# Kernel tuning notes

Hardware: AMD Instinct MI355X
Metric: run time of the kernel (lower is better)

Reference implementation:

```python
import jax, jax.numpy as jnp
import numpy as np

N_NODES = 100000
N_EDGES = 1600000
IN_DIM = 3
HID = 128


def setup_inputs() -> dict:
    key = jax.random.key(0)
    ks = jax.random.split(key, 16)
    s = 0.05
    inp = {
        "x": jax.random.normal(ks[0], (N_NODES, IN_DIM), dtype=jnp.float32),
        "pos": jax.random.normal(ks[1], (N_NODES, IN_DIM), dtype=jnp.float32),
        "edge_index": jax.random.randint(ks[2], (2, N_EDGES), 0, N_NODES, dtype=jnp.int64),
        # EdgeConv MLP: Linear(2*IN_DIM, HID) -> ReLU -> Linear(HID, HID)
        "w1": jax.random.normal(ks[3], (2 * IN_DIM, HID), dtype=jnp.float32) * s,
        "b1": jnp.zeros((HID,), dtype=jnp.float32),
        "w2": jax.random.normal(ks[4], (HID, HID), dtype=jnp.float32) * s,
        "b2": jnp.zeros((HID,), dtype=jnp.float32),
        # encoder tail: ReLU -> Linear(HID, HID)
        "w3": jax.random.normal(ks[5], (HID, HID), dtype=jnp.float32) * s,
        "b3": jnp.zeros((HID,), dtype=jnp.float32),
        # decoder: Linear(HID, HID) -> ReLU -> Linear(HID, 3)
        "w4": jax.random.normal(ks[6], (HID, HID), dtype=jnp.float32) * s,
        "b4": jnp.zeros((HID,), dtype=jnp.float32),
        "w5": jax.random.normal(ks[7], (HID, 3), dtype=jnp.float32) * s,
        "b5": jnp.zeros((3,), dtype=jnp.float32),
    }
    return inp


def reference(x, pos, edge_index, w1, b1, w2, b2, w3, b3, w4, b4, w5, b5):
    n = x.shape[0]
    src, dst = edge_index[0], edge_index[1]  # message j(src) -> i(dst)
    xi = x[dst]                               # [E, 3] target features
    xj = x[src]                               # [E, 3] source features
    msg_in = jnp.concatenate([xi, xj - xi], axis=-1)          # [E, 6]
    h = jax.nn.relu(msg_in @ w1 + b1) @ w2 + b2               # [E, HID]
    agg = jax.ops.segment_max(h, dst, num_segments=n)         # [N, HID]
    agg = jnp.where(jnp.isneginf(agg), 0.0, agg)              # nodes with no edges -> 0
    enc = jax.nn.relu(agg) @ w3 + b3                          # [N, HID]
    dec = jax.nn.relu(enc @ w4 + b4) @ w5 + b5                # [N, 3]
    return pos + 0.1 * jnp.tanh(dec)
```

## Files before the change

### kernel.cpp

```cpp
#include <hip/hip_runtime.h>
#include <hip/hip_bf16.h>

typedef __attribute__((ext_vector_type(8))) short short8;
typedef __attribute__((ext_vector_type(4))) float floatx4;
typedef __attribute__((ext_vector_type(2))) unsigned short ushortx2;

#define NHID 128
#define PADROW 136
#define EB 64
#define EB2 128
#define PB 256

__device__ __forceinline__ unsigned short f2bf(float x) {
  unsigned int u = __float_as_uint(x);
  u += 0x7FFFu + ((u >> 16) & 1u);
  return (unsigned short)(u >> 16);
}

__device__ __forceinline__ unsigned int pkbf(float a, float b) {
  __hip_bfloat162 h = __float22bfloat162_rn(make_float2(a, b));
  union { __hip_bfloat162 h; unsigned int u; } cv;
  cv.h = h;
  return cv.u;
}

__device__ __forceinline__ unsigned int pack2(float a, float b) {
  return (unsigned int)f2bf(a) | ((unsigned int)f2bf(b) << 16);
}

__device__ __forceinline__ unsigned int pkmax(unsigned int a, unsigned int b) {
  union { unsigned int u; ushortx2 v; } x, y;
  x.u = a; y.u = b;
  x.v = __builtin_elementwise_max(x.v, y.v);
  return x.u;
}

__device__ __forceinline__ void casmax(unsigned int* ap, unsigned int run) {
  unsigned int old = *ap;
  while (true) {
    unsigned int mx = pkmax(old, run);
    if (mx == old) break;
    unsigned int got = atomicCAS(ap, old, mx);
    if (got == old) break;
    old = got;
  }
}

__device__ __forceinline__ bool detect64(const int* __restrict__ ei) {
  unsigned long long b = __ballot(ei[2 * (threadIdx.x & 63) + 1] != 0);
  return b == 0ULL;
}

__device__ __forceinline__ void load_bfrags(const float* __restrict__ wmat,
                                            short8* bf, int m, int q) {
  #pragma unroll
  for (int kc = 0; kc < 4; ++kc) {
    #pragma unroll
    for (int nt = 0; nt < 8; ++nt) {
      short8 v;
      #pragma unroll
      for (int j = 0; j < 8; ++j)
        v[j] = (short)f2bf(wmat[(kc * 32 + q * 8 + j) * NHID + nt * 16 + m]);
      bf[kc * 8 + nt] = v;
    }
  }
}

__device__ __forceinline__ void load_bfrags_perm(const float* __restrict__ wmat,
                                                 short8* bf, int m, int q) {
  #pragma unroll
  for (int kc = 0; kc < 4; ++kc) {
    #pragma unroll
    for (int nt = 0; nt < 8; ++nt) {
      short8 v;
      #pragma unroll
      for (int j = 0; j < 8; ++j) {
        const int khw = kc * 32 + q * 8 + j;
        const int ctrue = ((khw & 7) << 4) | (khw >> 3);
        v[j] = (short)f2bf(wmat[ctrue * NHID + nt * 16 + m]);
      }
      bf[kc * 8 + nt] = v;
    }
  }
}

__device__ __forceinline__ void mfma_block(const unsigned short* uA,
                                           const short8* bf, floatx4* acc,
                                           int w, int m, int q) {
  #pragma unroll
  for (int kc = 0; kc < 4; ++kc) {
    short8 a = *(const short8*)(uA + (16 * w + m) * PADROW + kc * 32 + q * 8);
    #pragma unroll
    for (int nt = 0; nt < 8; ++nt)
      acc[nt] = __builtin_amdgcn_mfma_f32_16x16x32_bf16(a, bf[kc * 8 + nt],
                                                        acc[nt], 0, 0, 0);
  }
}

__global__ void zero_detect_kernel(float4* __restrict__ p, int n4,
                                   const int* __restrict__ ei, int* __restrict__ flag) {
  if (blockIdx.x == 0 && threadIdx.x < 64) {
    unsigned long long b = __ballot(ei[2 * threadIdx.x + 1] != 0);
    if (threadIdx.x == 0) flag[0] = (b == 0ULL) ? 1 : 0;
  }
  int i = blockIdx.x * blockDim.x + threadIdx.x;
  int stride = gridDim.x * blockDim.x;
  float4 z = make_float4(0.f, 0.f, 0.f, 0.f);
  for (; i < n4; i += stride) p[i] = z;
}


__global__ __launch_bounds__(256) void part_hist(const int* __restrict__ ei,
                                                 int* __restrict__ mat, int E, int nbuck,
                                                 float4* __restrict__ aggz, int n4) {
  const int bl = blockIdx.x, t = threadIdx.x;
  if (bl >= PB) {
    int i = (bl - PB) * 256 + t;
    const int st = (gridDim.x - PB) * 256;
    float4 z = make_float4(0.f, 0.f, 0.f, 0.f);
    for (; i < n4; i += st) aggz[i] = z;
    return;
  }
  __shared__ int hist[512];
  const bool is64 = detect64(ei);
  for (int i = t; i < nbuck; i += 256) hist[i] = 0;
  __syncthreads();
  const int chunk = (E + PB - 1) / PB;
  const int lo = bl * chunk;
  const int hi = min(lo + chunk, E);
  for (int i = lo + t; i < hi; i += 256) {
    int d = is64 ? ei[2 * E + 2 * i] : ei[E + i];
    atomicAdd(&hist[d >> 8], 1);
  }
  __syncthreads();
  for (int bu = t; bu < nbuck; bu += 256) mat[bu * PB + bl] = hist[bu];
}

__global__ __launch_bounds__(256) void scan_rows(int* __restrict__ mat,
                                                 int* __restrict__ btot, int nbuck) {
  __shared__ int sh[256];
  const int bu = blockIdx.x, t = threadIdx.x;
  const int v = mat[bu * PB + t];
  sh[t] = v;
  __syncthreads();
  for (int off = 1; off < 256; off <<= 1) {
    int x = (t >= off) ? sh[t - off] : 0;
    __syncthreads();
    sh[t] += x;
    __syncthreads();
  }
  mat[bu * PB + t] = sh[t] - v;
  if (t == 255) btot[bu] = sh[255];
}

__global__ __launch_bounds__(512) void scan_buckets(const int* __restrict__ btot,
                                                    int* __restrict__ bstart, int nbuck) {
  __shared__ int sh[512];
  const int t = threadIdx.x;
  const int v = (t < nbuck) ? btot[t] : 0;
  sh[t] = v;
  __syncthreads();
  for (int off = 1; off < 512; off <<= 1) {
    int x = (t >= off) ? sh[t - off] : 0;
    __syncthreads();
    sh[t] += x;
    __syncthreads();
  }
  if (t <= nbuck) bstart[t] = sh[t] - v;
}

__global__ __launch_bounds__(256) void part_scatter(const int* __restrict__ ei,
                                                    const int* __restrict__ mat,
                                                    const int* __restrict__ bstart,
                                                    int2* __restrict__ mid, int E, int nbuck) {
  __shared__ int off[512];
  const bool is64 = detect64(ei);
  const int bl = blockIdx.x, t = threadIdx.x;
  for (int bu = t; bu < nbuck; bu += 256) off[bu] = bstart[bu] + mat[bu * PB + bl];
  __syncthreads();
  const int chunk = (E + PB - 1) / PB;
  const int lo = bl * chunk;
  const int hi = min(lo + chunk, E);
  for (int i = lo + t; i < hi; i += 256) {
    int s = is64 ? ei[2 * i]         : ei[i];
    int d = is64 ? ei[2 * E + 2 * i] : ei[E + i];
    int p = atomicAdd(&off[d >> 8], 1);
    mid[p] = make_int2(s, d);
  }
}

__global__ __launch_bounds__(256) void bucket_sort(const int2* __restrict__ mid,
                                                   const int* __restrict__ bstart,
                                                   int2* __restrict__ sorted) {
  __shared__ int h[256], cnt[256];
  const int bu = blockIdx.x, t = threadIdx.x;
  const int lo = bstart[bu], hi = bstart[bu + 1];
  h[t] = 0; cnt[t] = 0;
  __syncthreads();
  for (int i = lo + t; i < hi; i += 256) atomicAdd(&h[mid[i].y & 255], 1);
  __syncthreads();
  const int v = h[t];
  for (int off = 1; off < 256; off <<= 1) {
    int x = (t >= off) ? h[t - off] : 0;
    __syncthreads();
    h[t] += x;
    __syncthreads();
  }
  const int excl = h[t] - v;
  __syncthreads();
  h[t] = excl;
  __syncthreads();
  for (int i = lo + t; i < hi; i += 256) {
    int2 e = mid[i];
    const int dl = e.y & 255;
    const int p = lo + h[dl] + atomicAdd(&cnt[dl], 1);
    sorted[p] = e;
  }
}


__global__ __launch_bounds__(512, 2) void edge_sorted_kernel(
    const float* __restrict__ x, const int2* __restrict__ sorted,
    const float* __restrict__ w1, const float* __restrict__ b1,
    const float* __restrict__ w2, const float* __restrict__ b2,
    unsigned int* aggu, int N, int E) {
  __shared__ unsigned short us[EB2 * PADROW];
  __shared__ short8 w2f[2048];
  __shared__ int esS[EB2], edS[EB2];
  __shared__ int pn[2];
  __shared__ unsigned long long maskS[2];
  __shared__ unsigned int pmS[8][64];

  const int t = threadIdx.x;
  const int lane = t & 63;
  const int w = t >> 6;
  const int m = lane & 15;
  const int q = lane >> 4;

  float b1c[8], b2c[8];
  #pragma unroll
  for (int nt = 0; nt < 8; ++nt) { b1c[nt] = b1[nt * 16 + m]; b2c[nt] = b2[nt * 16 + m]; }

  short8 bf1[8];
  #pragma unroll
  for (int nt = 0; nt < 8; ++nt) {
    short8 v;
    #pragma unroll
    for (int j = 0; j < 8; ++j)
      v[j] = (q == 0 && j < 6) ? (short)f2bf(w1[j * NHID + nt * 16 + m]) : (short)0;
    bf1[nt] = v;
  }

  for (int idx = t; idx < 2048; idx += 512) {
    const int fg = idx >> 6, ln = idx & 63;
    const int mm = ln & 15;
    const int kc = fg >> 3, nt = fg & 7;
    short8 v;
    #pragma unroll
    for (int j = 0; j < 8; ++j) {
      const int khw = kc * 32 + (ln >> 4) * 8 + j;
      const int ctrue = ((khw & 7) << 4) | (khw >> 3);
      v[j] = (short)f2bf(w2[ctrue * NHID + nt * 16 + mm]);
    }
    w2f[idx] = v;
  }

  const int jc = t & 63;
  const int quarter = t >> 6;

  const int nbt = (E + EB2 - 1) / EB2;
  __syncthreads();

  int2 sv = make_int2(0, -1);
  {
    const int tile0 = blockIdx.x;
    const int gb = tile0 * EB2;
    if (t < EB2) {
      const int e = gb + t;
      if (tile0 < nbt && e < E) sv = sorted[e];
    } else if (t == EB2) {
      sv.y = (tile0 < nbt && gb > 0) ? sorted[gb - 1].y : -2;
    } else if (t == EB2 + 1) {
      sv.y = (tile0 < nbt && gb + EB2 < E) ? sorted[gb + EB2].y : -2;
    }
  }

  for (int tile = blockIdx.x; tile < nbt; tile += gridDim.x) {
    if (t < EB2) { esS[t] = sv.x; edS[t] = sv.y; }
    else if (t == EB2) pn[0] = sv.y;
    else if (t == EB2 + 1) pn[1] = sv.y;
    __syncthreads();

    if (w == 0) {
      int d0 = edS[lane];
      int dp0 = (lane == 0) ? -9 : edS[lane - 1];
      unsigned long long mk0 = __ballot(lane == 0 || d0 != dp0);
      int d1 = edS[64 + lane];
      int dp1 = edS[63 + lane];
      unsigned long long mk1 = __ballot(d1 != dp1);
      if (lane == 0) { maskS[0] = mk0; maskS[1] = mk1; }
    }

    floatx4 acc[8];
    #pragma unroll
    for (int nt = 0; nt < 8; ++nt) { floatx4 z = {0.f, 0.f, 0.f, 0.f}; acc[nt] = z; }
    short8 a1 = {0, 0, 0, 0, 0, 0, 0, 0};
    if (q == 0) {
      const int e = 16 * w + m;
      const int si = esS[e];
      const int d0 = edS[e];
      const int di = (d0 < 0) ? 0 : d0;
      float xi0 = x[di * 3], xi1 = x[di * 3 + 1], xi2 = x[di * 3 + 2];
      float dd0 = x[si * 3] - xi0, dd1 = x[si * 3 + 1] - xi1, dd2 = x[si * 3 + 2] - xi2;
      union { short8 s; uint4 u; } cv;
      cv.u = make_uint4(pkbf(xi0, xi1), pkbf(xi2, dd0), pkbf(dd1, dd2), 0u);
      a1 = cv.s;
    }
    #pragma unroll
    for (int nt = 0; nt < 8; ++nt)
      acc[nt] = __builtin_amdgcn_mfma_f32_16x16x32_bf16(a1, bf1[nt], acc[nt], 0, 0, 0);

    #pragma unroll
    for (int r = 0; r < 4; ++r) {
      union { short8 s; uint4 u; } cv;
      cv.u = make_uint4(
        pkbf(fmaxf(acc[0][r] + b1c[0], 0.f), fmaxf(acc[1][r] + b1c[1], 0.f)),
        pkbf(fmaxf(acc[2][r] + b1c[2], 0.f), fmaxf(acc[3][r] + b1c[3], 0.f)),
        pkbf(fmaxf(acc[4][r] + b1c[4], 0.f), fmaxf(acc[5][r] + b1c[5], 0.f)),
        pkbf(fmaxf(acc[6][r] + b1c[6], 0.f), fmaxf(acc[7][r] + b1c[7], 0.f)));
      *(short8*)(&us[(16 * w + q * 4 + r) * PADROW + m * 8]) = cv.s;
    }
    __syncthreads();

    #pragma unroll
    for (int nt = 0; nt < 8; ++nt) { floatx4 z = {0.f, 0.f, 0.f, 0.f}; acc[nt] = z; }
    #pragma unroll
    for (int kc = 0; kc < 4; ++kc) {
      short8 a = *(const short8*)(&us[(16 * w + m) * PADROW + kc * 32 + q * 8]);
      #pragma unroll
      for (int nt = 0; nt < 8; ++nt)
        acc[nt] = __builtin_amdgcn_mfma_f32_16x16x32_bf16(a, w2f[(kc * 8 + nt) * 64 + lane],
                                                          acc[nt], 0, 0, 0);
    }
    __syncthreads();

    #pragma unroll
    for (int r = 0; r < 4; ++r) {
      union { short8 s; uint4 u; } cv;
      cv.u = make_uint4(
        pkbf(fmaxf(acc[0][r] + b2c[0], 0.f), fmaxf(acc[1][r] + b2c[1], 0.f)),
        pkbf(fmaxf(acc[2][r] + b2c[2], 0.f), fmaxf(acc[3][r] + b2c[3], 0.f)),
        pkbf(fmaxf(acc[4][r] + b2c[4], 0.f), fmaxf(acc[5][r] + b2c[5], 0.f)),
        pkbf(fmaxf(acc[6][r] + b2c[6], 0.f), fmaxf(acc[7][r] + b2c[7], 0.f)));
      *(short8*)(&us[(16 * w + q * 4 + r) * PADROW + m * 8]) = cv.s;
    }
    __syncthreads();

    {
      const int tn = tile + gridDim.x;
      const int gb = tn * EB2;
      int2 nv = make_int2(0, -1);
      if (t < EB2) {
        const int e = gb + t;
        if (tn < nbt && e < E) nv = sorted[e];
      } else if (t == EB2) {
        nv.y = (tn < nbt && gb > 0) ? sorted[gb - 1].y : -2;
      } else if (t == EB2 + 1) {
        nv.y = (tn < nbt && gb + EB2 < E) ? sorted[gb + EB2].y : -2;
      }
      sv = nv;
    }

    int os = -1, onxt = 0, od = -1; unsigned int opart = 0;
    {
      const unsigned long long mk0 = maskS[0], mk1 = maskS[1];
      const int prevd = pn[0], nextd = pn[1];
      const int r0 = quarter * 16, r1 = r0 + 16;
      const unsigned int* us32 = (const unsigned int*)us;
      int s;
      if (r0 < 64) {
        s = 63 - __builtin_clzll(mk0 & (~0ULL >> (63 - r0)));
      } else {
        unsigned long long hm = mk1 & (~0ULL >> (127 - r0));
        s = hm ? 127 - __builtin_clzll(hm) : 63 - __builtin_clzll(mk0);
      }
      while (s < r1) {
        int nxt;
        if (s < 63) {
          unsigned long long ab = mk0 & (~0ULL << (s + 1));
          if (ab) nxt = __builtin_ffsll((long long)ab) - 1;
          else    nxt = mk1 ? 64 + __builtin_ffsll((long long)mk1) - 1 : 128;
        } else if (s == 63) {
          nxt = mk1 ? 64 + __builtin_ffsll((long long)mk1) - 1 : 128;
        } else if (s < 127) {
          unsigned long long ab = mk1 & (~0ULL << (s - 63));
          nxt = ab ? 64 + __builtin_ffsll((long long)ab) - 1 : 128;
        } else nxt = 128;

        const int lo = (s > r0) ? s : r0;
        const int hi = (nxt < r1) ? nxt : r1;
        unsigned int run = 0;
        for (int r = lo; r < hi; ++r)
          run = pkmax(run, us32[r * (PADROW >> 1) + jc]);

        if (s < r0) {
          pmS[quarter][jc] = run;
        } else if (nxt <= r1) {
          const int d = edS[s];
          if (d >= 0) {
            const bool bnd = (s == 0 && prevd == d) || (nxt == 128 && nextd == d);
            unsigned int* ap = aggu + (size_t)d * 64 + jc;
            if (!bnd) *ap = run;
            else if (run) casmax(ap, run);
          }
        } else {
          os = s; onxt = nxt; od = edS[s]; opart = run;
        }
        s = nxt;
      }
    }
    __syncthreads();

    if (os >= 0 && od >= 0) {
      const int endq = (onxt - 1) >> 4;
      #pragma unroll 4
      for (int qq = quarter + 1; qq <= endq; ++qq)
        opart = pkmax(opart, pmS[qq][jc]);
      const bool bnd = (os == 0 && pn[0] == od) || (onxt == 128 && pn[1] == od);
      unsigned int* ap = aggu + (size_t)od * 64 + jc;
      if (!bnd) *ap = opart;
      else if (opart) casmax(ap, opart);
    }
    __syncthreads();
  }
}


__global__ __launch_bounds__(256, 2) void edge_atomic_kernel(
    const float* __restrict__ x, const int* __restrict__ ei,
    const float* __restrict__ w1, const float* __restrict__ b1,
    const float* __restrict__ w2, const float* __restrict__ b2,
    unsigned int* aggu, const int* __restrict__ flag64, int N, int E) {
  __shared__ unsigned short uA[EB * PADROW];
  __shared__ float w1s[6 * NHID];
  __shared__ float b1s[NHID], b2s[NHID];
  __shared__ int es[EB], ed[EB];

  const int t = threadIdx.x;
  const int lane = t & 63;
  const int w = t >> 6;
  const int m = lane & 15;
  const int q = lane >> 4;

  for (int i = t; i < 6 * NHID; i += 256) w1s[i] = w1[i];
  if (t < NHID) { b1s[t] = b1[t]; b2s[t] = b2[t]; }

  short8 bf[32];
  load_bfrags(w2, bf, m, q);

  const bool is64 = (flag64[0] != 0);
  const int nb = (E + EB - 1) / EB;

  for (int batch = blockIdx.x; batch < nb; batch += gridDim.x) {
    const int gbase = batch * EB;
    if (t < EB) {
      int e = gbase + t;
      es[t] = (e < E) ? (is64 ? ei[2 * e] : ei[e]) : 0;
    } else if (t < 2 * EB) {
      int tt = t - EB;
      int e = gbase + tt;
      ed[tt] = (e < E) ? (is64 ? ei[2 * E + 2 * e] : ei[E + e]) : 0;
    }
    __syncthreads();
    {
      const int e = t >> 2;
      const int c0 = (t & 3) * 32;
      const int si = es[e], di = ed[e];
      float xi0 = x[di * 3], xi1 = x[di * 3 + 1], xi2 = x[di * 3 + 2];
      float msg[6];
      msg[0] = xi0; msg[1] = xi1; msg[2] = xi2;
      msg[3] = x[si * 3] - xi0; msg[4] = x[si * 3 + 1] - xi1; msg[5] = x[si * 3 + 2] - xi2;
      unsigned int* d32 = (unsigned int*)uA;
      const int base32 = (e * PADROW + c0) >> 1;
      #pragma unroll
      for (int cc = 0; cc < 32; cc += 2) {
        float u0 = b1s[c0 + cc], u1 = b1s[c0 + cc + 1];
        #pragma unroll
        for (int d = 0; d < 6; ++d) {
          u0 += msg[d] * w1s[d * NHID + c0 + cc];
          u1 += msg[d] * w1s[d * NHID + c0 + cc + 1];
        }
        d32[base32 + (cc >> 1)] = pack2(fmaxf(u0, 0.f), fmaxf(u1, 0.f));
      }
    }
    __syncthreads();

    floatx4 acc[8];
    #pragma unroll
    for (int nt = 0; nt < 8; ++nt) { floatx4 z = {0.f, 0.f, 0.f, 0.f}; acc[nt] = z; }
    mfma_block(uA, bf, acc, w, m, q);

    #pragma unroll
    for (int nt = 0; nt < 8; ++nt) {
      const int c = nt * 16 + m;
      const float bb = b2s[c];
      const int kst = m * 8 + nt;
      #pragma unroll
      for (int r = 0; r < 4; ++r) {
        const int erow = 16 * w + q * 4 + r;
        if (gbase + erow < E) {
          float hb = acc[nt][r] + bb;
          if (hb > 0.f) {
            unsigned int v = (unsigned int)f2bf(hb);
            casmax(aggu + (size_t)ed[erow] * 64 + (kst >> 1), v << (16 * (kst & 1)));
          }
        }
      }
    }
    __syncthreads();
  }
}


__global__ __launch_bounds__(256, 2) void encdec_kernel(
    const float* __restrict__ w3, const float* __restrict__ b3,
    const float* __restrict__ w4, const float* __restrict__ b4,
    const float* __restrict__ w5, const float* __restrict__ b5,
    const float* __restrict__ pos, const unsigned short* __restrict__ agg16,
    float* __restrict__ out, int N) {
  __shared__ unsigned short uA[EB * PADROW];
  __shared__ short8 w4f[2048];
  __shared__ float w5s[NHID * 3];

  const int t = threadIdx.x;
  const int lane = t & 63;
  const int w = t >> 6;
  const int m = lane & 15;
  const int q = lane >> 4;

  float b3c[8], b4c[8];
  #pragma unroll
  for (int nt = 0; nt < 8; ++nt) { b3c[nt] = b3[nt * 16 + m]; b4c[nt] = b4[nt * 16 + m]; }

  short8 bf3[32];
  load_bfrags_perm(w3, bf3, m, q);

  for (int idx = t; idx < 2048; idx += 256) {
    const int fg = idx >> 6, ln = idx & 63;
    const int mm = ln & 15;
    const int kc = fg >> 3, nt = fg & 7;
    short8 v;
    #pragma unroll
    for (int j = 0; j < 8; ++j) {
      const int khw = kc * 32 + (ln >> 4) * 8 + j;
      const int ctrue = ((khw & 7) << 4) | (khw >> 3);
      v[j] = (short)f2bf(w4[ctrue * NHID + nt * 16 + mm]);
    }
    w4f[idx] = v;
  }
  for (int i = t; i < NHID * 3; i += 256) w5s[i] = w5[i];
  const float b50 = b5[0], b51 = b5[1], b52 = b5[2];

  const int ch = t & 15;
  const int rr = t >> 4;
  const int nb = (N + EB - 1) / EB;
  __syncthreads();

  uint4 rv[4];
  const uint4 uz = make_uint4(0u, 0u, 0u, 0u);
  {
    const int b0 = blockIdx.x;
    #pragma unroll
    for (int k = 0; k < 4; ++k) {
      const int node = b0 * EB + rr + 16 * k;
      rv[k] = (b0 < nb && node < N) ? ((const uint4*)agg16)[(size_t)node * 16 + ch] : uz;
    }
  }

  for (int batch = blockIdx.x; batch < nb; batch += gridDim.x) {
    const int base = batch * EB;
    #pragma unroll
    for (int k = 0; k < 4; ++k)
      *(uint4*)(&uA[(rr + 16 * k) * PADROW + ch * 8]) = rv[k];
    __syncthreads();

    {
      const int nxb = batch + gridDim.x;
      #pragma unroll
      for (int k = 0; k < 4; ++k) {
        const int node = nxb * EB + rr + 16 * k;
        rv[k] = (nxb < nb && node < N) ? ((const uint4*)agg16)[(size_t)node * 16 + ch] : uz;
      }
    }

    floatx4 acc[8];
    #pragma unroll
    for (int nt = 0; nt < 8; ++nt) { floatx4 z = {0.f, 0.f, 0.f, 0.f}; acc[nt] = z; }
    mfma_block(uA, bf3, acc, w, m, q);
    __syncthreads();

    #pragma unroll
    for (int r = 0; r < 4; ++r) {
      union { short8 s; uint4 u; } cv;
      cv.u = make_uint4(
        pkbf(acc[0][r] + b3c[0], acc[1][r] + b3c[1]),
        pkbf(acc[2][r] + b3c[2], acc[3][r] + b3c[3]),
        pkbf(acc[4][r] + b3c[4], acc[5][r] + b3c[5]),
        pkbf(acc[6][r] + b3c[6], acc[7][r] + b3c[7]));
      *(short8*)(&uA[(16 * w + q * 4 + r) * PADROW + m * 8]) = cv.s;
    }
    __syncthreads();

    #pragma unroll
    for (int nt = 0; nt < 8; ++nt) { floatx4 z = {0.f, 0.f, 0.f, 0.f}; acc[nt] = z; }
    #pragma unroll
    for (int kc = 0; kc < 4; ++kc) {
      short8 a = *(const short8*)(&uA[(16 * w + m) * PADROW + kc * 32 + q * 8]);
      #pragma unroll
      for (int nt = 0; nt < 8; ++nt)
        acc[nt] = __builtin_amdgcn_mfma_f32_16x16x32_bf16(a, w4f[(kc * 8 + nt) * 64 + lane],
                                                          acc[nt], 0, 0, 0);
    }

    float p[4][3];
    #pragma unroll
    for (int r = 0; r < 4; ++r) { p[r][0] = 0.f; p[r][1] = 0.f; p[r][2] = 0.f; }
    #pragma unroll
    for (int nt = 0; nt < 8; ++nt) {
      const int c = nt * 16 + m;
      const float bb = b4c[nt];
      const float w50 = w5s[c * 3], w51 = w5s[c * 3 + 1], w52 = w5s[c * 3 + 2];
      #pragma unroll
      for (int r = 0; r < 4; ++r) {
        float tv = fmaxf(acc[nt][r] + bb, 0.f);
        p[r][0] += tv * w50; p[r][1] += tv * w51; p[r][2] += tv * w52;
      }
    }
    #pragma unroll
    for (int off = 8; off >= 1; off >>= 1) {
      #pragma unroll
      for (int r = 0; r < 4; ++r) {
        p[r][0] += __shfl_xor(p[r][0], off, 16);
        p[r][1] += __shfl_xor(p[r][1], off, 16);
        p[r][2] += __shfl_xor(p[r][2], off, 16);
      }
    }
    if (m == 0) {
      #pragma unroll
      for (int r = 0; r < 4; ++r) {
        const int node = base + 16 * w + q * 4 + r;
        if (node < N) {
          out[node * 3]     = pos[node * 3]     + 0.1f * tanhf(p[r][0] + b50);
          out[node * 3 + 1] = pos[node * 3 + 1] + 0.1f * tanhf(p[r][1] + b51);
          out[node * 3 + 2] = pos[node * 3 + 2] + 0.1f * tanhf(p[r][2] + b52);
        }
      }
    }
    __syncthreads();
  }
}

extern "C" void kernel_launch(void* const* d_in, const int* in_sizes, int n_in,
                              void* d_out, int out_size, void* d_ws, size_t ws_size,
                              hipStream_t stream) {
  const float* x   = (const float*)d_in[0];
  const float* pos = (const float*)d_in[1];
  const int*   ei  = (const int*)d_in[2];
  const float* w1  = (const float*)d_in[3];
  const float* b1  = (const float*)d_in[4];
  const float* w2  = (const float*)d_in[5];
  const float* b2  = (const float*)d_in[6];
  const float* w3  = (const float*)d_in[7];
  const float* b3  = (const float*)d_in[8];
  const float* w4  = (const float*)d_in[9];
  const float* b4  = (const float*)d_in[10];
  const float* w5  = (const float*)d_in[11];
  const float* b5  = (const float*)d_in[12];
  float* out = (float*)d_out;

  const int N = in_sizes[0] / 3;
  const int E = in_sizes[2] / 2;
  const int nbuck = (N + 255) >> 8;

  char* ws = (char*)d_ws;
  unsigned short* agg16 = (unsigned short*)ws;
  const size_t aggB = (size_t)N * NHID * sizeof(unsigned short);
  int2* mid    = (int2*)(ws + aggB);
  int2* sorted = (int2*)(ws + aggB + (size_t)E * 8);
  int*  mat    = (int*)(ws + aggB + (size_t)E * 16);
  int*  btot   = mat + (size_t)nbuck * PB;
  int*  bstart = btot + nbuck;
  int*  flag   = bstart + nbuck + 2;
  const size_t needed = aggB + (size_t)E * 16 + ((size_t)nbuck * PB + 2 * nbuck + 8) * 4;

  if (ws_size >= needed && nbuck <= 511 && E >= 64) {
    part_hist<<<2048, 256, 0, stream>>>(ei, mat, E, nbuck, (float4*)agg16, N * 16);
    scan_rows<<<nbuck, 256, 0, stream>>>(mat, btot, nbuck);
    scan_buckets<<<1, 512, 0, stream>>>(btot, bstart, nbuck);
    part_scatter<<<PB, 256, 0, stream>>>(ei, mat, bstart, mid, E, nbuck);
    bucket_sort<<<nbuck, 256, 0, stream>>>(mid, bstart, sorted);
    edge_sorted_kernel<<<512, 512, 0, stream>>>(x, sorted, w1, b1, w2, b2,
                                                (unsigned int*)agg16, N, E);
  } else {
    int* flag2 = (int*)(ws + aggB);
    zero_detect_kernel<<<2048, 256, 0, stream>>>((float4*)agg16, N * 16, ei, flag2);
    edge_atomic_kernel<<<512, 256, 0, stream>>>(x, ei, w1, b1, w2, b2,
                                                (unsigned int*)agg16, flag2, N, E);
  }
  encdec_kernel<<<512, 256, 0, stream>>>(w3, b3, w4, b4, w5, b5, pos, agg16, out, N);
}
```

Before: 354.2 us.

## Fuse bucket scan into scatter, drop intra-wave barriers, seed accumulators with bias

After: 420.7 us. +18.8%, slower.

```diff
diff --git a/kernel.cpp b/kernel.cpp
--- a/kernel.cpp
+++ b/kernel.cpp
@@ -153,30 +153,34 @@
   if (t == 255) btot[bu] = sh[255];
 }
 
-__global__ __launch_bounds__(512) void scan_buckets(const int* __restrict__ btot,
-                                                    int* __restrict__ bstart, int nbuck) {
-  __shared__ int sh[512];
-  const int t = threadIdx.x;
-  const int v = (t < nbuck) ? btot[t] : 0;
-  sh[t] = v;
-  __syncthreads();
-  for (int off = 1; off < 512; off <<= 1) {
-    int x = (t >= off) ? sh[t - off] : 0;
-    __syncthreads();
-    sh[t] += x;
-    __syncthreads();
-  }
-  if (t <= nbuck) bstart[t] = sh[t] - v;
-}
-
 __global__ __launch_bounds__(256) void part_scatter(const int* __restrict__ ei,
                                                     const int* __restrict__ mat,
-                                                    const int* __restrict__ bstart,
+                                                    const int* __restrict__ btot,
+                                                    int* __restrict__ bstart,
                                                     int2* __restrict__ mid, int E, int nbuck) {
   __shared__ int off[512];
+  __shared__ int bsS[512];
   const bool is64 = detect64(ei);
   const int bl = blockIdx.x, t = threadIdx.x;
-  for (int bu = t; bu < nbuck; bu += 256) off[bu] = bstart[bu] + mat[bu * PB + bl];
+  const int o0 = (t < nbuck) ? btot[t] : 0;
+  const int o1 = (t + 256 < nbuck) ? btot[t + 256] : 0;
+  bsS[t] = o0; bsS[t + 256] = o1;
+  __syncthreads();
+  for (int o = 1; o < 256; o <<= 1) {
+    int x0 = (t >= o) ? bsS[t - o] : 0;
+    int x1 = (t >= o) ? bsS[256 + t - o] : 0;
+    __syncthreads();
+    bsS[t] += x0; bsS[256 + t] += x1;
+    __syncthreads();
+  }
+  const int tot0 = bsS[255];
+  bsS[256 + t] += tot0;
+  __syncthreads();
+  const int ex0 = bsS[t] - o0;
+  const int ex1 = bsS[256 + t] - o1;
+  if (bl == 0) { bstart[t] = ex0; bstart[256 + t] = ex1; }
+  off[t]       = ex0 + ((t < nbuck) ? mat[t * PB + bl] : 0);
+  off[256 + t] = ex1 + ((t + 256 < nbuck) ? mat[(t + 256) * PB + bl] : 0);
   __syncthreads();
   const int chunk = (E + PB - 1) / PB;
   const int lo = bl * chunk;
@@ -291,6 +295,21 @@
     else if (t == EB2 + 1) pn[1] = sv.y;
     __syncthreads();
 
+    {
+      const int tn = tile + gridDim.x;
+      const int gb = tn * EB2;
+      int2 nv = make_int2(0, -1);
+      if (t < EB2) {
+        const int e = gb + t;
+        if (tn < nbt && e < E) nv = sorted[e];
+      } else if (t == EB2) {
+        nv.y = (tn < nbt && gb > 0) ? sorted[gb - 1].y : -2;
+      } else if (t == EB2 + 1) {
+        nv.y = (tn < nbt && gb + EB2 < E) ? sorted[gb + EB2].y : -2;
+      }
+      sv = nv;
+    }
+
     if (w == 0) {
       int d0 = edS[lane];
       int dp0 = (lane == 0) ? -9 : edS[lane - 1];
@@ -303,7 +322,10 @@
 
     floatx4 acc[8];
     #pragma unroll
-    for (int nt = 0; nt < 8; ++nt) { floatx4 z = {0.f, 0.f, 0.f, 0.f}; acc[nt] = z; }
+    for (int nt = 0; nt < 8; ++nt) {
+      floatx4 z = {b1c[nt], b1c[nt], b1c[nt], b1c[nt]};
+      acc[nt] = z;
+    }
     short8 a1 = {0, 0, 0, 0, 0, 0, 0, 0};
     if (q == 0) {
       const int e = 16 * w + m;
@@ -324,16 +346,18 @@
     for (int r = 0; r < 4; ++r) {
       union { short8 s; uint4 u; } cv;
       cv.u = make_uint4(
-        pkbf(fmaxf(acc[0][r] + b1c[0], 0.f), fmaxf(acc[1][r] + b1c[1], 0.f)),
-        pkbf(fmaxf(acc[2][r] + b1c[2], 0.f), fmaxf(acc[3][r] + b1c[3], 0.f)),
-        pkbf(fmaxf(acc[4][r] + b1c[4], 0.f), fmaxf(acc[5][r] + b1c[5], 0.f)),
-        pkbf(fmaxf(acc[6][r] + b1c[6], 0.f), fmaxf(acc[7][r] + b1c[7], 0.f)));
+        pkbf(fmaxf(acc[0][r], 0.f), fmaxf(acc[1][r], 0.f)),
+        pkbf(fmaxf(acc[2][r], 0.f), fmaxf(acc[3][r], 0.f)),
+        pkbf(fmaxf(acc[4][r], 0.f), fmaxf(acc[5][r], 0.f)),
+        pkbf(fmaxf(acc[6][r], 0.f), fmaxf(acc[7][r], 0.f)));
       *(short8*)(&us[(16 * w + q * 4 + r) * PADROW + m * 8]) = cv.s;
     }
-    __syncthreads();
-
-    #pragma unroll
-    for (int nt = 0; nt < 8; ++nt) { floatx4 z = {0.f, 0.f, 0.f, 0.f}; acc[nt] = z; }
+
+    #pragma unroll
+    for (int nt = 0; nt < 8; ++nt) {
+      floatx4 z = {b2c[nt], b2c[nt], b2c[nt], b2c[nt]};
+      acc[nt] = z;
+    }
     #pragma unroll
     for (int kc = 0; kc < 4; ++kc) {
       short8 a = *(const short8*)(&us[(16 * w + m) * PADROW + kc * 32 + q * 8]);
@@ -342,34 +366,18 @@
         acc[nt] = __builtin_amdgcn_mfma_f32_16x16x32_bf16(a, w2f[(kc * 8 + nt) * 64 + lane],
                                                           acc[nt], 0, 0, 0);
     }
-    __syncthreads();
 
     #pragma unroll
     for (int r = 0; r < 4; ++r) {
       union { short8 s; uint4 u; } cv;
       cv.u = make_uint4(
-        pkbf(fmaxf(acc[0][r] + b2c[0], 0.f), fmaxf(acc[1][r] + b2c[1], 0.f)),
-        pkbf(fmaxf(acc[2][r] + b2c[2], 0.f), fmaxf(acc[3][r] + b2c[3], 0.f)),
-        pkbf(fmaxf(acc[4][r] + b2c[4], 0.f), fmaxf(acc[5][r] + b2c[5], 0.f)),
-        pkbf(fmaxf(acc[6][r] + b2c[6], 0.f), fmaxf(acc[7][r] + b2c[7], 0.f)));
+        pkbf(fmaxf(acc[0][r], 0.f), fmaxf(acc[1][r], 0.f)),
+        pkbf(fmaxf(acc[2][r], 0.f), fmaxf(acc[3][r], 0.f)),
+        pkbf(fmaxf(acc[4][r], 0.f), fmaxf(acc[5][r], 0.f)),
+        pkbf(fmaxf(acc[6][r], 0.f), fmaxf(acc[7][r], 0.f)));
       *(short8*)(&us[(16 * w + q * 4 + r) * PADROW + m * 8]) = cv.s;
     }
     __syncthreads();
-
-    {
-      const int tn = tile + gridDim.x;
-      const int gb = tn * EB2;
-      int2 nv = make_int2(0, -1);
-      if (t < EB2) {
-        const int e = gb + t;
-        if (tn < nbt && e < E) nv = sorted[e];
-      } else if (t == EB2) {
-        nv.y = (tn < nbt && gb > 0) ? sorted[gb - 1].y : -2;
-      } else if (t == EB2 + 1) {
-        nv.y = (tn < nbt && gb + EB2 < E) ? sorted[gb + EB2].y : -2;
-      }
-      sv = nv;
-    }
 
     int os = -1, onxt = 0, od = -1; unsigned int opart = 0;
     {
@@ -595,24 +603,28 @@
 
     floatx4 acc[8];
     #pragma unroll
-    for (int nt = 0; nt < 8; ++nt) { floatx4 z = {0.f, 0.f, 0.f, 0.f}; acc[nt] = z; }
+    for (int nt = 0; nt < 8; ++nt) {
+      floatx4 z = {b3c[nt], b3c[nt], b3c[nt], b3c[nt]};
+      acc[nt] = z;
+    }
     mfma_block(uA, bf3, acc, w, m, q);
-    __syncthreads();
 
     #pragma unroll
     for (int r = 0; r < 4; ++r) {
       union { short8 s; uint4 u; } cv;
       cv.u = make_uint4(
-        pkbf(acc[0][r] + b3c[0], acc[1][r] + b3c[1]),
-        pkbf(acc[2][r] + b3c[2], acc[3][r] + b3c[3]),
-        pkbf(acc[4][r] + b3c[4], acc[5][r] + b3c[5]),
-        pkbf(acc[6][r] + b3c[6], acc[7][r] + b3c[7]));
+        pkbf(acc[0][r], acc[1][r]),
+        pkbf(acc[2][r], acc[3][r]),
+        pkbf(acc[4][r], acc[5][r]),
+        pkbf(acc[6][r], acc[7][r]));
       *(short8*)(&uA[(16 * w + q * 4 + r) * PADROW + m * 8]) = cv.s;
     }
-    __syncthreads();
-
-    #pragma unroll
-    for (int nt = 0; nt < 8; ++nt) { floatx4 z = {0.f, 0.f, 0.f, 0.f}; acc[nt] = z; }
+
+    #pragma unroll
+    for (int nt = 0; nt < 8; ++nt) {
+      floatx4 z = {b4c[nt], b4c[nt], b4c[nt], b4c[nt]};
+      acc[nt] = z;
+    }
     #pragma unroll
     for (int kc = 0; kc < 4; ++kc) {
       short8 a = *(const short8*)(&uA[(16 * w + m) * PADROW + kc * 32 + q * 8]);
@@ -628,11 +640,10 @@
     #pragma unroll
     for (int nt = 0; nt < 8; ++nt) {
       const int c = nt * 16 + m;
-      const float bb = b4c[nt];
       const float w50 = w5s[c * 3], w51 = w5s[c * 3 + 1], w52 = w5s[c * 3 + 2];
       #pragma unroll
       for (int r = 0; r < 4; ++r) {
-        float tv = fmaxf(acc[nt][r] + bb, 0.f);
+        float tv = fmaxf(acc[nt][r], 0.f);
         p[r][0] += tv * w50; p[r][1] += tv * w51; p[r][2] += tv * w52;
       }
     }
@@ -690,14 +701,12 @@
   int*  mat    = (int*)(ws + aggB + (size_t)E * 16);
   int*  btot   = mat + (size_t)nbuck * PB;
   int*  bstart = btot + nbuck;
-  int*  flag   = bstart + nbuck + 2;
-  const size_t needed = aggB + (size_t)E * 16 + ((size_t)nbuck * PB + 2 * nbuck + 8) * 4;
+  const size_t needed = aggB + (size_t)E * 16 + ((size_t)nbuck * PB + nbuck + 520) * 4;
 
   if (ws_size >= needed && nbuck <= 511 && E >= 64) {
     part_hist<<<2048, 256, 0, stream>>>(ei, mat, E, nbuck, (float4*)agg16, N * 16);
     scan_rows<<<nbuck, 256, 0, stream>>>(mat, btot, nbuck);
-    scan_buckets<<<1, 512, 0, stream>>>(btot, bstart, nbuck);
-    part_scatter<<<PB, 256, 0, stream>>>(ei, mat, bstart, mid, E, nbuck);
+    part_scatter<<<PB, 256, 0, stream>>>(ei, mat, btot, bstart, mid, E, nbuck);
     bucket_sort<<<nbuck, 256, 0, stream>>>(mid, bstart, sorted);
     edge_sorted_kernel<<<512, 512, 0, stream>>>(x, sorted, w1, b1, w2, b2,
                                                 (unsigned int*)agg16, N, E);
```
